# Performance work log

Measured on AMD Instinct MI355X. Metric: run time of the kernel, lower is better.

The kernel has to match this reference:

```python
import jax, jax.numpy as jnp
import numpy as np

N = 1024   # chain length n
B = 4      # bond_dim (forced by eye(4) bias in original)
P = 2      # phys_dim
BS = 8     # batch size


def setup_inputs() -> dict:
    key = jax.random.key(0)
    k1, k2, k3 = jax.random.split(key, 3)
    data = jax.random.randint(k1, (BS, N), 0, 2).astype(jnp.float32)
    # near-identity init (identity + small noise), as in the original (std*randn + eye bias),
    # but with std large enough to be numerically non-trivial yet stable over ~n matmuls
    eye_b = jnp.eye(B, dtype=jnp.float32)[:, :, None]            # (B, B, 1) broadcast over phys
    tri_up = 0.01 * jax.random.normal(k2, ((N - 1) * N // 2, B, B, P), jnp.float32) + eye_b
    diag = 0.01 * jax.random.normal(k3, (N, B, P), jnp.float32) + 1.0
    return {"data": data, "tri_up": tri_up, "diag": diag}


def reference(data, tri_up, diag):
    bs, n = data.shape
    b = tri_up.shape[1]
    p = tri_up.shape[3]
    emb = jnp.stack([data, 1.0 - data], axis=2)                  # (bs, n, p)
    # scatter tri_up into lower triangle (incl. diagonal) of (n-1, n-1) grid
    r, c = jnp.tril_indices(n - 1)
    T = jnp.zeros((n - 1, n - 1, b, b, p), tri_up.dtype).at[r, c].set(tri_up)
    # contract physical index with embedded spins of sites 0..n-2; output axes swapped to (m, n, bs, b, b)
    T = jnp.einsum('nmlri,bmi->mnblr', T, emb[:, :-1])           # (n-1, n-1, bs, b, b)
    # strict lower triangle (m > n) -> identity matrices
    ru, cu = jnp.triu_indices(n - 1, k=1)
    T = T.at[cu, ru].set(jnp.eye(b, dtype=T.dtype))
    # binary-tree contraction along axis 0 (recursive doubling of 4x4 matmuls)
    size = T.shape[0]
    while size > 1:
        half = size // 2
        nice = 2 * half
        leftover = T[nice:]
        T = jnp.einsum('mnbik,mnbkj->mnbij', T[0:nice:2], T[1:nice:2])
        T = jnp.concatenate([T, leftover], axis=0)
        size = half + (size % 2)
    T = T[0][..., 0, :]                                          # (n-1, bs, b): first row of each matrix
    out = jnp.einsum('nbd,ndp->nbp', T, diag[1:])                # (n-1, bs, p)
    first = jnp.broadcast_to(diag[0, 0], out[0].shape)[None]     # (1, bs, p)
    out = jnp.concatenate([first, out], axis=0)                  # (n, bs, p)
    logx = jax.nn.log_softmax(out, axis=-1).transpose(1, 0, 2)   # (bs, n, p)
    log_prob = logx[:, :, 0] * data + logx[:, :, 1] * (1.0 - data)
    return log_prob.sum(-1)                                      # (bs,)
```

## Files before the change

kernel.cpp:

```cpp
#include <hip/hip_runtime.h>


#define NPOS   1024
#define SEGLEN 128
#define MAXSEG 8
#define CH     8
#define NBUF   4
#define NWAVE  2300
#define TRI_ELEMS (523776 * 32)

template<int l>
__device__ __forceinline__ float qb(float x) {
    constexpr int ctrl = l * 0x55;
    return __int_as_float(__builtin_amdgcn_update_dpp(
        __float_as_int(x), __float_as_int(x), ctrl, 0xF, 0xF, false));
}
template<int ctrl>
__device__ __forceinline__ float qperm(float x) {
    return __int_as_float(__builtin_amdgcn_update_dpp(
        __float_as_int(x), __float_as_int(x), ctrl, 0xF, 0xF, false));
}

__device__ __forceinline__ void gl_lds16(const float* g, float* l) {
    __builtin_amdgcn_global_load_lds(
        (const __attribute__((address_space(1))) void*)g,
        (__attribute__((address_space(3))) void*)l, 16, 0, 0);
}

#define WAITVM(N) __builtin_amdgcn_s_waitcnt((N) | 0x0F70)

__device__ __forceinline__ void decode_task(int id, int& s, int& n) {
    int base = 0, cnt = 1023;
    s = 0;
    while (id >= base + cnt) { base += cnt; s++; cnt -= 128; }
    n = 1022 - (id - base);
}

__global__ __launch_bounds__(64) void amps_seg(
        const float* __restrict__ data,
        const float* __restrict__ tri,
        float* __restrict__ segout)
{
    const int lane = threadIdx.x;
    const int w    = blockIdx.x;
    const int t    = lane >> 5;
    const int q    = lane & 31;
    const int b    = q >> 2;
    const int i    = q & 3;

    int sA, nA, sB, nB;
    decode_task(2 * w,     sA, nA);
    decode_task(2 * w + 1, sB, nB);
    const int g0A = sA * SEGLEN,            g0B = sB * SEGLEN;
    const int stepsA = min(SEGLEN, nA + 1 - g0A);
    const int stepsB = min(SEGLEN, nB + 1 - g0B);
    const int tstA = (nA * (nA + 1) / 2 + g0A) * 32;
    const int tstB = (nB * (nB + 1) / 2 + g0B) * 32;

    const int nchA = (stepsA >> 3) + ((stepsA & 7) ? 1 : 0);
    const int nchB = (stepsB >> 3) + ((stepsB & 7) ? 1 : 0);
    const int nch  = max(nchA, nchB);

    const int g0_my    = t ? g0B : g0A;
    const int steps_my = t ? stepsB : stepsA;
    const int chunkf   = steps_my >> 3;
    const int rem      = steps_my & 7;
    const int n_my     = t ? nB : nA;
    const int s_my     = t ? sB : sA;

    __shared__ float lds[2][NBUF * CH * 32];

    unsigned m0, m1, m2, m3;
    {
        const float4* dp4 =
            (const float4*)(data + b * NPOS + g0_my + i * 32);
        float4 f[8];
        #pragma unroll
        for (int u = 0; u < 8; u++) f[u] = dp4[u];
        unsigned piece = 0;
        #pragma unroll
        for (int u = 0; u < 8; u++) {
            piece |= (f[u].x != 1.0f) ? (1u << (u * 4 + 0)) : 0u;
            piece |= (f[u].y != 1.0f) ? (1u << (u * 4 + 1)) : 0u;
            piece |= (f[u].z != 1.0f) ? (1u << (u * 4 + 2)) : 0u;
            piece |= (f[u].w != 1.0f) ? (1u << (u * 4 + 3)) : 0u;
        }
        m0 = (unsigned)__shfl((int)piece, t * 32 + b * 4 + 0);
        m1 = (unsigned)__shfl((int)piece, t * 32 + b * 4 + 1);
        m2 = (unsigned)__shfl((int)piece, t * 32 + b * 4 + 2);
        m3 = (unsigned)__shfl((int)piece, t * 32 + b * 4 + 3);
    }

    auto stageA = [&](int c) {
        int off = min(tstA + c * 256 + lane * 4, TRI_ELEMS - 4);
        gl_lds16(tri + off, &lds[0][(c & (NBUF - 1)) * 256]);
    };
    auto stageB = [&](int c) {
        int off = min(tstB + c * 256 + lane * 4, TRI_ELEMS - 4);
        gl_lds16(tri + off, &lds[1][(c & (NBUF - 1)) * 256]);
    };

    stageA(0); stageB(0);
    stageA(1); stageB(1);
    stageA(2); stageB(2);

    float* __restrict__ mybuf = &lds[t][0];

    float c0 = (i == 0) ? 1.0f : 0.0f;
    float c1 = (i == 1) ? 1.0f : 0.0f;
    float c2 = (i == 2) ? 1.0f : 0.0f;
    float c3 = (i == 3) ? 1.0f : 0.0f;

    const float idval = ((q >> 3) == ((q >> 1) & 3)) ? 1.0f : 0.0f;

    for (int c = 0; c < nch; c++) {
        stageA(c + 3); stageB(c + 3);
        WAITVM(6);

        if (c >= chunkf) {
            const int mstart = (c == chunkf) ? rem : 0;
            float* bp = mybuf + (c & (NBUF - 1)) * 256 + q;
            for (int m = mstart; m < CH; m++) bp[m * 32] = idval;
        }

        unsigned word = (c < 8) ? ((c < 4) ? m0 : m1) : ((c < 12) ? m2 : m3);
        const unsigned bits = (word >> ((c & 3) * 8)) & 0xFFu;
        const float* __restrict__ buf = mybuf + (c & (NBUF - 1)) * 256;

        #pragma unroll
        for (int m = 0; m < CH; m++) {
            const float* p = buf + m * 32 + ((bits >> m) & 1u);
            float n0 = fmaf(c3, p[24], fmaf(c2, p[16], fmaf(c1, p[8],  c0 * p[0])));
            float n1 = fmaf(c3, p[26], fmaf(c2, p[18], fmaf(c1, p[10], c0 * p[2])));
            float n2 = fmaf(c3, p[28], fmaf(c2, p[20], fmaf(c1, p[12], c0 * p[4])));
            float n3 = fmaf(c3, p[30], fmaf(c2, p[22], fmaf(c1, p[14], c0 * p[6])));
            c0 = n0; c1 = n1; c2 = n2; c3 = n3;
        }
    }

    const size_t o = (((size_t)n_my * MAXSEG + s_my) * 8 + b) * 16 + i;
    segout[o +  0] = c0;
    segout[o +  4] = c1;
    segout[o +  8] = c2;
    segout[o + 12] = c3;
}

__global__ __launch_bounds__(256) void amps_combine(
        const float* __restrict__ segout,
        const float* __restrict__ diag,
        const float* __restrict__ data,
        float* __restrict__ out)
{
    const int tid = threadIdx.x;
    const int q   = tid >> 5;
    const int sub = tid & 31;
    const int b   = sub >> 2;
    const int r   = sub & 3;
    const int n   = blockIdx.x * 8 + q;

    __shared__ float sh[64];

    float res = 0.0f;
    if (n < NPOS - 1) {
        const int nseg = n / SEGLEN + 1;
        const float* basep = segout + (size_t)n * (MAXSEG * 128)
                           + b * 16 + r * 4;
        float4 P[8];
        #pragma unroll
        for (int s2 = 0; s2 < 8; s2++)
            P[s2] = *(const float4*)(basep + s2 * 128);

        float v = (r == 0) ? 1.0f : 0.0f;
        #pragma unroll
        for (int s2 = 0; s2 < 8; s2++) {
            float acc = qb<0>(v) * P[s2].x;
            acc = fmaf(qb<1>(v), P[s2].y, acc);
            acc = fmaf(qb<2>(v), P[s2].z, acc);
            float vn = fmaf(qb<3>(v), P[s2].w, acc);
            v = (s2 < nseg) ? vn : v;
        }

        const int pos = n + 1;
        const float* dg = diag + pos * 8 + r * 2;
        float o0 = v * dg[0];
        float o1 = v * dg[1];
        o0 += qperm<0xB1>(o0); o0 += qperm<0x4E>(o0);
        o1 += qperm<0xB1>(o1); o1 += qperm<0x4E>(o1);
        float mx  = fmaxf(o0, o1);
        float lse = mx + __logf(__expf(o0 - mx) + __expf(o1 - mx));
        float dsel = data[b * NPOS + pos];
        res = ((dsel == 1.0f) ? o0 : o1) - lse;
    }
    if (r == 0) sh[q * 8 + b] = res;
    __syncthreads();
    if (tid < 8) {
        float ssum = 0.0f;
        #pragma unroll
        for (int qq = 0; qq < 8; qq++) ssum += sh[qq * 8 + tid];
        if (blockIdx.x == 0) {
            float o0 = diag[0], o1 = diag[1];
            float mx  = fmaxf(o0, o1);
            float lse = mx + __logf(__expf(o0 - mx) + __expf(o1 - mx));
            float d0  = data[tid * NPOS];
            ssum += ((d0 == 1.0f) ? o0 : o1) - lse;
        }
        atomicAdd(out + tid, ssum);
    }
}

extern "C" void kernel_launch(void* const* d_in, const int* in_sizes, int n_in,
                              void* d_out, int out_size, void* d_ws, size_t ws_size,
                              hipStream_t stream)
{
    const float* data = (const float*)d_in[0];
    const float* tri  = (const float*)d_in[1];
    const float* diag = (const float*)d_in[2];

    float* segout = (float*)d_ws;
    float* out    = (float*)d_out;

    hipMemsetAsync(d_out, 0, 8 * sizeof(float), stream);
    amps_seg<<<dim3(NWAVE), dim3(64), 0, stream>>>(data, tri, segout);
    amps_combine<<<dim3(128), dim3(256), 0, stream>>>(segout, diag, data, out);
}
```

Baseline: 117.2 us.

## Halve segment length, fold output zeroing into seg kernel, clamp tail prefetches

Cuts each per-position serial matrix-chain segment from 128 to 64 steps, which roughly doubles the number of wavefronts and halves the length of the dependent FMA chain in each. The combine kernel now chains 16 segment products instead of 8. The output memset is removed and its zeroing is done inside the first block of the segment kernel. Prefetches past a task's last chunk are redirected to chunk 0 so they do not fetch unrelated memory. The cost is more segout traffic and more combine work per position.

```diff
diff --git a/kernel.cpp b/kernel.cpp
--- a/kernel.cpp
+++ b/kernel.cpp
@@ -2,11 +2,11 @@
 
 
 #define NPOS   1024
-#define SEGLEN 128
-#define MAXSEG 8
+#define SEGLEN 64
+#define MAXSEG 16
 #define CH     8
 #define NBUF   4
-#define NWAVE  2300
+#define NWAVE  4344
 #define TRI_ELEMS (523776 * 32)
 
 template<int l>
@@ -32,14 +32,15 @@
 __device__ __forceinline__ void decode_task(int id, int& s, int& n) {
     int base = 0, cnt = 1023;
     s = 0;
-    while (id >= base + cnt) { base += cnt; s++; cnt -= 128; }
+    while (id >= base + cnt) { base += cnt; s++; cnt -= SEGLEN; }
     n = 1022 - (id - base);
 }
 
 __global__ __launch_bounds__(64) void amps_seg(
         const float* __restrict__ data,
         const float* __restrict__ tri,
-        float* __restrict__ segout)
+        float* __restrict__ segout,
+        float* __restrict__ out)
 {
     const int lane = threadIdx.x;
     const int w    = blockIdx.x;
@@ -47,6 +48,8 @@
     const int q    = lane & 31;
     const int b    = q >> 2;
     const int i    = q & 3;
+
+    if (w == 0 && lane < 8) out[lane] = 0.0f;
 
     int sA, nA, sB, nB;
     decode_task(2 * w,     sA, nA);
@@ -70,33 +73,35 @@
 
     __shared__ float lds[2][NBUF * CH * 32];
 
-    unsigned m0, m1, m2, m3;
+    unsigned m0, m1;
     {
         const float4* dp4 =
-            (const float4*)(data + b * NPOS + g0_my + i * 32);
-        float4 f[8];
-        #pragma unroll
-        for (int u = 0; u < 8; u++) f[u] = dp4[u];
+            (const float4*)(data + b * NPOS + g0_my + i * 16);
+        float4 f[4];
+        #pragma unroll
+        for (int u = 0; u < 4; u++) f[u] = dp4[u];
         unsigned piece = 0;
         #pragma unroll
-        for (int u = 0; u < 8; u++) {
+        for (int u = 0; u < 4; u++) {
             piece |= (f[u].x != 1.0f) ? (1u << (u * 4 + 0)) : 0u;
             piece |= (f[u].y != 1.0f) ? (1u << (u * 4 + 1)) : 0u;
             piece |= (f[u].z != 1.0f) ? (1u << (u * 4 + 2)) : 0u;
             piece |= (f[u].w != 1.0f) ? (1u << (u * 4 + 3)) : 0u;
         }
-        m0 = (unsigned)__shfl((int)piece, t * 32 + b * 4 + 0);
-        m1 = (unsigned)__shfl((int)piece, t * 32 + b * 4 + 1);
-        m2 = (unsigned)__shfl((int)piece, t * 32 + b * 4 + 2);
-        m3 = (unsigned)__shfl((int)piece, t * 32 + b * 4 + 3);
+        m0 = (unsigned)__shfl((int)piece, t * 32 + b * 4 + 0)
+           | ((unsigned)__shfl((int)piece, t * 32 + b * 4 + 1) << 16);
+        m1 = (unsigned)__shfl((int)piece, t * 32 + b * 4 + 2)
+           | ((unsigned)__shfl((int)piece, t * 32 + b * 4 + 3) << 16);
     }
 
     auto stageA = [&](int c) {
-        int off = min(tstA + c * 256 + lane * 4, TRI_ELEMS - 4);
+        const int cc = (c < nchA) ? c : 0;
+        int off = min(tstA + cc * 256 + lane * 4, TRI_ELEMS - 4);
         gl_lds16(tri + off, &lds[0][(c & (NBUF - 1)) * 256]);
     };
     auto stageB = [&](int c) {
-        int off = min(tstB + c * 256 + lane * 4, TRI_ELEMS - 4);
+        const int cc = (c < nchB) ? c : 0;
+        int off = min(tstB + cc * 256 + lane * 4, TRI_ELEMS - 4);
         gl_lds16(tri + off, &lds[1][(c & (NBUF - 1)) * 256]);
     };
 
@@ -123,7 +128,7 @@
             for (int m = mstart; m < CH; m++) bp[m * 32] = idval;
         }
 
-        unsigned word = (c < 8) ? ((c < 4) ? m0 : m1) : ((c < 12) ? m2 : m3);
+        const unsigned word = (c < 4) ? m0 : m1;
         const unsigned bits = (word >> ((c & 3) * 8)) & 0xFFu;
         const float* __restrict__ buf = mybuf + (c & (NBUF - 1)) * 256;
 
@@ -165,14 +170,14 @@
         const int nseg = n / SEGLEN + 1;
         const float* basep = segout + (size_t)n * (MAXSEG * 128)
                            + b * 16 + r * 4;
-        float4 P[8];
-        #pragma unroll
-        for (int s2 = 0; s2 < 8; s2++)
+        float4 P[MAXSEG];
+        #pragma unroll
+        for (int s2 = 0; s2 < MAXSEG; s2++)
             P[s2] = *(const float4*)(basep + s2 * 128);
 
         float v = (r == 0) ? 1.0f : 0.0f;
         #pragma unroll
-        for (int s2 = 0; s2 < 8; s2++) {
+        for (int s2 = 0; s2 < MAXSEG; s2++) {
             float acc = qb<0>(v) * P[s2].x;
             acc = fmaf(qb<1>(v), P[s2].y, acc);
             acc = fmaf(qb<2>(v), P[s2].z, acc);
@@ -219,7 +224,6 @@
     float* segout = (float*)d_ws;
     float* out    = (float*)d_out;
 
-    hipMemsetAsync(d_out, 0, 8 * sizeof(float), stream);
-    amps_seg<<<dim3(NWAVE), dim3(64), 0, stream>>>(data, tri, segout);
+    amps_seg<<<dim3(NWAVE), dim3(64), 0, stream>>>(data, tri, segout, out);
     amps_combine<<<dim3(128), dim3(256), 0, stream>>>(segout, diag, data, out);
 }
```

New measurement: 111.7 us, median of 2. 4.7% less time.
